# Kernel optimization log

Measured on AMD Instinct MI355X. Metric: run time of the kernel, lower is better.

Reference implementation:

```python
import jax, jax.numpy as jnp
import numpy as np

MIN_STD = 1e-05
LEAKY_SLOPE = 0.01


def setup_inputs() -> dict:
    key = jax.random.key(0)
    ks = jax.random.split(key, 8)
    T, B, F, H, A = 512, 256, 64, 256, 8
    s_in = 1.0 / np.sqrt(F)
    s_h = 1.0 / np.sqrt(H)
    return {
        "x": jax.random.normal(ks[0], (T, B, F), jnp.float32),
        "dones": jax.random.randint(ks[1], (T, B), 0, 2, jnp.int32),
        "W1": jax.random.normal(ks[2], (H, F), jnp.float32) * s_in,
        "b1": jnp.zeros((H,), jnp.float32),
        "W_ih": jax.random.normal(ks[3], (3 * H, H), jnp.float32) * s_h,
        "W_hh": jax.random.normal(ks[4], (3 * H, H), jnp.float32) * s_h,
        "b_ih": jnp.zeros((3 * H,), jnp.float32),
        "b_hh": jnp.zeros((3 * H,), jnp.float32),
        "Wm": jax.random.normal(ks[5], (A, H), jnp.float32) * s_h,
        "bm": jnp.zeros((A,), jnp.float32),
        "Ws": jax.random.normal(ks[6], (A, H), jnp.float32) * s_h,
        "bs": jnp.zeros((A,), jnp.float32),
    }


def reference(x, dones, W1, b1, W_ih, W_hh, b_ih, b_hh, Wm, bm, Ws, bs):
    T, B, _ = x.shape
    H = W1.shape[0]

    # shared_net: Linear + LeakyReLU, applied to the whole [T,B,F] tensor
    sf = jnp.einsum('tbf,hf->tbh', x, W1) + b1
    sf = jnp.where(sf >= 0, sf, LEAKY_SLOPE * sf)

    # per-timestep GRU with done-masked hidden reset (PyTorch gate order r,z,n)
    def step(h, inp):
        f_t, d_t = inp                      # f_t: [B,H], d_t: [B]
        h = jnp.where(d_t[:, None] > 0, 0.0, h)
        gi = f_t @ W_ih.T + b_ih            # [B,3H]
        gh = h @ W_hh.T + b_hh              # [B,3H]
        r = jax.nn.sigmoid(gi[:, :H] + gh[:, :H])
        z = jax.nn.sigmoid(gi[:, H:2 * H] + gh[:, H:2 * H])
        n = jnp.tanh(gi[:, 2 * H:] + r * gh[:, 2 * H:])
        h_new = (1.0 - z) * n + z * h
        return h_new, h_new

    h0 = jnp.zeros((B, H), x.dtype)
    h_final, outs = jax.lax.scan(step, h0, (sf, dones))

    # Faithful to source: heads applied to the LAST step's gru_output [1,B,H]
    last = outs[-1][None]                   # [1,B,H]
    means = jnp.tanh(jnp.einsum('sbh,ah->sba', last, Wm) + bm)
    stds = jax.nn.softplus(jnp.einsum('sbh,ah->sba', last, Ws) + bs)
    stds = jnp.maximum(stds, MIN_STD)
    hidden = h_final[None]                  # [num_layers=1, B, H]
    return means, stds, hidden
```

## Files before the change

### kernel.cpp

```cpp
#include <hip/hip_runtime.h>
#include <math.h>

typedef __attribute__((ext_vector_type(8))) _Float16 f16x8;
typedef __attribute__((ext_vector_type(4))) _Float16 f16x4;
typedef __attribute__((ext_vector_type(4))) float f32x4;

#define TT 512
#define BB 256
#define HH 256
#define AA 8

#define OFF_W1   0u
#define OFF_WIH  32768u
#define OFF_WHH  425984u
#define OFF_H    819200u
#define OFF_GI   1081344u
#define GSTRIDE  393216

__device__ inline float fexp2(float x) { return __builtin_amdgcn_exp2f(x); }
__device__ inline float frcp(float x)  { return __builtin_amdgcn_rcpf(x); }
__device__ inline float fsigm(float x) { return frcp(1.f + fexp2(x * -1.4426950408889634f)); }
__device__ inline float ftanh_(float x){ return 1.f - 2.f * frcp(1.f + fexp2(x * 2.8853900817779268f)); }

__global__ __launch_bounds__(256) void prepack(
    const float* __restrict__ W1, const float* __restrict__ Wih,
    const float* __restrict__ Whh, unsigned char* __restrict__ ws) {
  int gid = blockIdx.x * 256 + threadIdx.x;
  int wave = gid >> 6, l = gid & 63;
  const float* src; int K; int tix; size_t dst;
  if (wave < 32)       { src = W1;  K = 64;  tix = wave;       dst = OFF_W1; }
  else if (wave < 416) { src = Wih; K = 256; tix = wave - 32;  dst = OFF_WIH; }
  else                 { src = Whh; K = 256; tix = wave - 416; dst = OFF_WHH; }
  int ntJ = (K == 64) ? 16 : 48;
  int kt = tix / ntJ, jt = tix % ntJ;
  int j;
  if (K == 64) j = jt * 16 + (l & 15);
  else { int g = jt % 3, blk = jt / 3; j = g * 256 + blk * 16 + (l & 15); }
  int k = kt * 32 + (l >> 4) * 8;
  const float* p = src + (size_t)j * K + k;
  f16x8 frag;
#pragma unroll
  for (int e = 0; e < 8; ++e) frag[e] = (_Float16)p[e];
  *(f16x8*)(ws + dst + ((size_t)tix * 64 + l) * 16) = frag;
}

__global__ __launch_bounds__(256) void gru_gi(
    const float* __restrict__ x, const float* __restrict__ b1,
    const float* __restrict__ b_ih, const float* __restrict__ b_hh,
    const unsigned char* __restrict__ wsro, unsigned char* __restrict__ giout,
    int t0) {
  __shared__ __align__(16) _Float16 sfh[2][16 * 256];
  int tid = threadIdx.x, w = tid >> 6, l = tid & 63;
  int tp = blockIdx.x >> 4, bt = blockIdx.x & 15;
  int row = l & 15, kg = l >> 4;

  const f16x8* pW1 = (const f16x8*)(wsro + OFF_W1);
#pragma unroll
  for (int tt = 0; tt < 2; ++tt) {
    int t = t0 + tp * 2 + tt;
    f32x4 sacc[4] = {{0.f,0.f,0.f,0.f},{0.f,0.f,0.f,0.f},{0.f,0.f,0.f,0.f},{0.f,0.f,0.f,0.f}};
    size_t xbase = ((size_t)t * BB + bt * 16 + row) * 64;
#pragma unroll
    for (int kt = 0; kt < 2; ++kt) {
      float4 p0 = *(const float4*)(x + xbase + kt * 32 + kg * 8);
      float4 p1 = *(const float4*)(x + xbase + kt * 32 + kg * 8 + 4);
      float xv[8] = {p0.x, p0.y, p0.z, p0.w, p1.x, p1.y, p1.z, p1.w};
      f16x8 xh;
#pragma unroll
      for (int e = 0; e < 8; ++e) xh[e] = (_Float16)xv[e];
#pragma unroll
      for (int jj = 0; jj < 4; ++jj) {
        f16x8 bw = pW1[(kt * 16 + w * 4 + jj) * 64 + l];
        sacc[jj] = __builtin_amdgcn_mfma_f32_16x16x32_f16(xh, bw, sacc[jj], 0, 0, 0);
      }
    }
#pragma unroll
    for (int jj = 0; jj < 4; ++jj) {
      int j = (w * 4 + jj) * 16 + row;
      float b1v = b1[j];
#pragma unroll
      for (int rg = 0; rg < 4; ++rg) {
        int rr = kg * 4 + rg;
        float v = sacc[jj][rg] + b1v;
        v = v >= 0.f ? v : 0.01f * v;
        int byt = (j * 2) ^ ((rr & 7) << 4);
        *(_Float16*)((char*)sfh[tt] + rr * 512 + byt) = (_Float16)v;
      }
    }
  }
  __syncthreads();

  f32x4 gacc[2][12];
#pragma unroll
  for (int tt = 0; tt < 2; ++tt)
#pragma unroll
    for (int jj = 0; jj < 12; ++jj) gacc[tt][jj] = (f32x4){0.f, 0.f, 0.f, 0.f};
  const f16x8* pWih = (const f16x8*)(wsro + OFF_WIH);
  for (int kt = 0; kt < 8; ++kt) {
    int rb = row * 512 + ((kt * 64 + kg * 16) ^ ((row & 7) << 4));
    f16x8 ah0 = *(const f16x8*)((const char*)sfh[0] + rb);
    f16x8 ah1 = *(const f16x8*)((const char*)sfh[1] + rb);
#pragma unroll
    for (int jj = 0; jj < 12; ++jj) {
      f16x8 bw = pWih[((size_t)(kt * 48 + w * 12 + jj)) * 64 + l];
      gacc[0][jj] = __builtin_amdgcn_mfma_f32_16x16x32_f16(ah0, bw, gacc[0][jj], 0, 0, 0);
      gacc[1][jj] = __builtin_amdgcn_mfma_f32_16x16x32_f16(ah1, bw, gacc[1][jj], 0, 0, 0);
    }
  }
  float biasv[12];
#pragma unroll
  for (int jj = 0; jj < 12; ++jj) {
    int jt = w * 12 + jj;
    int g = jt % 3, blk = jt / 3;
    int j = g * 256 + blk * 16 + row;
    biasv[jj] = b_ih[j] + (g < 2 ? b_hh[j] : 0.f);
  }
#pragma unroll
  for (int tt = 0; tt < 2; ++tt) {
    unsigned char* gbase =
        giout + (size_t)((tp * 2 + tt) * 16 + bt) * 24576 + (l >> 5) * 12288;
#pragma unroll
    for (int jj = 0; jj < 12; ++jj) {
      int jt = w * 12 + jj;
      f16x4 o;
#pragma unroll
      for (int rg = 0; rg < 4; ++rg) o[rg] = (_Float16)(gacc[tt][jj][rg] + biasv[jj]);
      *(f16x4*)(gbase + jt * 256 + (l & 31) * 8) = o;
    }
  }
}

__global__ __launch_bounds__(512, 2) void gru_seq(
    const int* __restrict__ dones, const float* __restrict__ b_hh,
    const float* __restrict__ Wm, const float* __restrict__ bm,
    const float* __restrict__ Wsv, const float* __restrict__ bsv,
    const unsigned char* __restrict__ wsro, unsigned char* __restrict__ hcar,
    const unsigned char* __restrict__ gi, int t0, int tch,
    float* __restrict__ out) {
  __shared__ __align__(16) unsigned char hbuf[2][8192];
  __shared__ unsigned char dnb[2048];
  int tid = threadIdx.x, w = tid >> 6, u = tid & 63;
  int bt8 = blockIdx.x, bt16 = bt8 >> 1, half = bt8 & 1;
  int kg = u >> 4;
  int col16 = u & 15, rgrp = (u >> 4) & 1, blk = u >> 5;
  int c = (2 * w + blk) * 16 + col16;

  f16x8 whh[6][8];
  const f16x8* pWhh = (const f16x8*)(wsro + OFF_WHH);
#pragma unroll
  for (int jj = 0; jj < 6; ++jj)
#pragma unroll
    for (int kt = 0; kt < 8; ++kt)
      whh[jj][kt] = pWhh[(size_t)(kt * 48 + 6 * w + jj) * 64 + u];

  float bn = b_hh[512 + c];

  int ab0 = (kg * 256 + (u & 7) * 16) ^ (kg << 4);
  int ab1 = ab0 ^ 64;
  int ku2 = c >> 3, e2 = c & 7;
  int wbase = (ku2 * 256 + rgrp * 64 + e2 * 2) ^ ((ku2 & 7) << 4);
  const char* hro = (const char*)hbuf;

  {
    int buf = tid >> 8, r = tid & 255;
    f16x8 z;
#pragma unroll
    for (int e = 0; e < 8; ++e) z[e] = (_Float16)0.f;
    *(f16x8*)((char*)hbuf + buf * 8192 + (r >> 3) * 256 + 128 + (r & 7) * 16) = z;
  }

  float h_old[4];
#pragma unroll
  for (int rg = 0; rg < 4; ++rg) {
    float hv = ((const float*)hcar)[(bt8 * 8 + rgrp * 4 + rg) * 256 + c];
    h_old[rg] = hv;
    *(_Float16*)((char*)hbuf + (wbase ^ (rg << 4))) = (_Float16)hv;
  }

#pragma unroll
  for (int ii = 0; ii < 4; ++ii) {
    int ix = ii * 512 + tid;
    if (ix < tch * 8) {
      int ti = t0 + (ix >> 3) + 1;
      dnb[ix] = (ti < TT) ? (unsigned char)(dones[ti * BB + bt8 * 8 + (ix & 7)] != 0) : (unsigned char)0;
    }
  }

  const unsigned char* gpt = gi + (size_t)bt16 * 24576 + half * 12288 +
                             (2 * w + blk) * 768 + (u & 31) * 8;
  f16x4 gA[3], gB[3];
#pragma unroll
  for (int g = 0; g < 3; ++g) gA[g] = *(const f16x4*)(gpt + g * 256);

  asm volatile("s_waitcnt lgkmcnt(0)" ::: "memory");
  __builtin_amdgcn_s_barrier();

#define STEP(TL, P, GC, GN)                                                     \
  {                                                                             \
    int tn = (TL) + 1 < tch ? (TL) + 1 : tch - 1;                               \
    const unsigned char* gpn = gpt + (size_t)tn * GSTRIDE;                      \
    GN[0] = *(const f16x4*)(gpn);                                               \
    GN[1] = *(const f16x4*)(gpn + 256);                                         \
    GN[2] = *(const f16x4*)(gpn + 512);                                         \
    f32x4 acc[6];                                                               \
    _Pragma("unroll") for (int jj = 0; jj < 6; ++jj)                            \
        acc[jj] = (f32x4){0.f, 0.f, 0.f, 0.f};                                  \
    _Pragma("unroll") for (int kt = 0; kt < 8; ++kt) {                          \
      f16x8 ah = *(const f16x8*)(hro + (P) * 8192 + kt * 1024 +                 \
                                 ((kt & 1) ? ab1 : ab0));                       \
      _Pragma("unroll") for (int jj = 0; jj < 6; ++jj)                          \
        acc[jj] = __builtin_amdgcn_mfma_f32_16x16x32_f16(ah, whh[jj][kt],       \
                                                         acc[jj], 0, 0, 0);     \
    }                                                                           \
    int dn4 = *(const int*)(dnb + (TL) * 8 + rgrp * 4);                         \
    char* hw = (char*)hbuf + ((P) ^ 1) * 8192;                                  \
    _Pragma("unroll") for (int rg = 0; rg < 4; ++rg) {                          \
      float avr = blk ? acc[3][rg] : acc[0][rg];                                \
      float avz = blk ? acc[4][rg] : acc[1][rg];                                \
      float avn = blk ? acc[5][rg] : acc[2][rg];                                \
      float rs = fsigm((float)GC[0][rg] + avr);                                 \
      float zs = fsigm((float)GC[1][rg] + avz);                                 \
      float ng = ftanh_((float)GC[2][rg] + rs * (avn + bn));                    \
      float hn = ng + zs * (h_old[rg] - ng);                                    \
      hn = ((dn4 >> (rg * 8)) & 0xff) ? 0.f : hn;                               \
      h_old[rg] = hn;                                                           \
      *(_Float16*)(hw + (wbase ^ (rg << 4))) = (_Float16)hn;                    \
    }                                                                           \
    asm volatile("s_waitcnt lgkmcnt(0)" ::: "memory");                          \
    __builtin_amdgcn_s_barrier();                                               \
  }

  for (int tl = 0; tl < tch; tl += 2) {
    STEP(tl, 0, gA, gB);
    STEP(tl + 1, 1, gB, gA);
  }
#undef STEP

#pragma unroll
  for (int rg = 0; rg < 4; ++rg)
    ((float*)hcar)[(bt8 * 8 + rgrp * 4 + rg) * 256 + c] = h_old[rg];

  if (t0 + tch == TT) {
#pragma unroll
    for (int rg = 0; rg < 4; ++rg)
      out[2 * BB * AA + (bt8 * 8 + rgrp * 4 + rg) * 256 + c] = h_old[rg];
    if (tid < 128) {
      int r2 = tid >> 4, a = (tid >> 1) & 7, hd = tid & 1;
      const float* W = hd ? Wsv : Wm;
      float acc2 = 0.f;
      for (int k = 0; k < 256; k += 8) {
        int ku = k >> 3;
        f16x8 vh = *(const f16x8*)(hro + ((ku * 256 + r2 * 16) ^ ((ku & 7) << 4)));
#pragma unroll
        for (int e = 0; e < 8; ++e)
          acc2 += (float)vh[e] * W[a * 256 + k + e];
      }
      int b = bt8 * 8 + r2;
      if (hd == 0) {
        out[b * AA + a] = tanhf(acc2 + bm[a]);
      } else {
        float v = acc2 + bsv[a];
        float sp = fmaxf(v, 0.f) + log1pf(expf(-fabsf(v)));
        out[BB * AA + b * AA + a] = fmaxf(sp, 1e-5f);
      }
    }
  }
}

extern "C" void kernel_launch(void* const* d_in, const int* in_sizes, int n_in,
                              void* d_out, int out_size, void* d_ws, size_t ws_size,
                              hipStream_t stream) {
  const float* x    = (const float*)d_in[0];
  const int*   dn   = (const int*)  d_in[1];
  const float* W1   = (const float*)d_in[2];
  const float* b1   = (const float*)d_in[3];
  const float* W_ih = (const float*)d_in[4];
  const float* W_hh = (const float*)d_in[5];
  const float* b_ih = (const float*)d_in[6];
  const float* b_hh = (const float*)d_in[7];
  const float* Wm   = (const float*)d_in[8];
  const float* bm   = (const float*)d_in[9];
  const float* Wsv  = (const float*)d_in[10];
  const float* bs   = (const float*)d_in[11];
  float* out = (float*)d_out;
  unsigned char* ws = (unsigned char*)d_ws;

  int tch = 256;
  while (tch > 1 && (size_t)OFF_GI + (size_t)tch * 16 * 24576 > ws_size) tch >>= 1;

  prepack<<<200, 256, 0, stream>>>(W1, W_ih, W_hh, ws);
  (void)hipMemsetAsync(ws + OFF_H, 0, 262144, stream);
  for (int t0 = 0; t0 < TT; t0 += tch) {
    gru_gi<<<dim3((tch / 2) * 16), 256, 0, stream>>>(x, b1, b_ih, b_hh, ws, ws + OFF_GI, t0);
    gru_seq<<<32, 512, 0, stream>>>(dn, b_hh, Wm, bm, Wsv, bs, ws, ws + OFF_H,
                                    ws + OFF_GI, t0, tch, out);
  }
}
```

Baseline: 791.3 us.

## Overlap next chunk's input GEMM with sequential GRU recurrence in fused kernel

The input projection kernel and the sequential GRU kernel are fused into one launch. The first 32 blocks run the recurrence for the current time chunk, while the extra blocks compute the input-gate projections for the next chunk into a double-buffered workspace. This hides the parallel GEMM work behind the latency-bound recurrence, which only occupies 32 blocks. The costs are a smaller chunk size, twice the workspace, and the GEMM blocks possibly competing with the recurrent blocks for memory bandwidth and CU resources.

```diff
diff --git a/kernel.cpp b/kernel.cpp
--- a/kernel.cpp
+++ b/kernel.cpp
@@ -44,17 +44,14 @@
   *(f16x8*)(ws + dst + ((size_t)tix * 64 + l) * 16) = frag;
 }
 
-__global__ __launch_bounds__(256) void gru_gi(
+__device__ __forceinline__ void gi_sf_phase(
     const float* __restrict__ x, const float* __restrict__ b1,
-    const float* __restrict__ b_ih, const float* __restrict__ b_hh,
-    const unsigned char* __restrict__ wsro, unsigned char* __restrict__ giout,
-    int t0) {
-  __shared__ __align__(16) _Float16 sfh[2][16 * 256];
-  int tid = threadIdx.x, w = tid >> 6, l = tid & 63;
-  int tp = blockIdx.x >> 4, bt = blockIdx.x & 15;
+    const unsigned char* __restrict__ wsro, _Float16* sfh0, _Float16* sfh1,
+    int t0, int tp, int bt, int tid) {
+  int w = tid >> 6, l = tid & 63;
   int row = l & 15, kg = l >> 4;
-
   const f16x8* pW1 = (const f16x8*)(wsro + OFF_W1);
+  _Float16* sfh[2] = {sfh0, sfh1};
 #pragma unroll
   for (int tt = 0; tt < 2; ++tt) {
     int t = t0 + tp * 2 + tt;
@@ -88,8 +85,15 @@
       }
     }
   }
-  __syncthreads();
-
+}
+
+__device__ __forceinline__ void gi_gemm_phase(
+    const float* __restrict__ b_ih, const float* __restrict__ b_hh,
+    const unsigned char* __restrict__ wsro, const _Float16* sfh0,
+    const _Float16* sfh1, unsigned char* __restrict__ giout,
+    int tp, int bt, int tid) {
+  int w = tid >> 6, l = tid & 63;
+  int row = l & 15, kg = l >> 4;
   f32x4 gacc[2][12];
 #pragma unroll
   for (int tt = 0; tt < 2; ++tt)
@@ -98,8 +102,8 @@
   const f16x8* pWih = (const f16x8*)(wsro + OFF_WIH);
   for (int kt = 0; kt < 8; ++kt) {
     int rb = row * 512 + ((kt * 64 + kg * 16) ^ ((row & 7) << 4));
-    f16x8 ah0 = *(const f16x8*)((const char*)sfh[0] + rb);
-    f16x8 ah1 = *(const f16x8*)((const char*)sfh[1] + rb);
+    f16x8 ah0 = *(const f16x8*)((const char*)sfh0 + rb);
+    f16x8 ah1 = *(const f16x8*)((const char*)sfh1 + rb);
 #pragma unroll
     for (int jj = 0; jj < 12; ++jj) {
       f16x8 bw = pWih[((size_t)(kt * 48 + w * 12 + jj)) * 64 + l];
@@ -130,16 +134,46 @@
   }
 }
 
-__global__ __launch_bounds__(512, 2) void gru_seq(
-    const int* __restrict__ dones, const float* __restrict__ b_hh,
+__global__ __launch_bounds__(256) void gru_gi(
+    const float* __restrict__ x, const float* __restrict__ b1,
+    const float* __restrict__ b_ih, const float* __restrict__ b_hh,
+    const unsigned char* __restrict__ wsro, unsigned char* __restrict__ giout,
+    int t0) {
+  __shared__ __align__(16) _Float16 sfh[2][16 * 256];
+  int tid = threadIdx.x;
+  int tp = blockIdx.x >> 4, bt = blockIdx.x & 15;
+  gi_sf_phase(x, b1, wsro, sfh[0], sfh[1], t0, tp, bt, tid);
+  __syncthreads();
+  gi_gemm_phase(b_ih, b_hh, wsro, sfh[0], sfh[1], giout, tp, bt, tid);
+}
+
+__global__ __launch_bounds__(512, 2) void gru_fused(
+    const float* __restrict__ x,
+    const int* __restrict__ dones, const float* __restrict__ b1,
+    const float* __restrict__ b_ih, const float* __restrict__ b_hh,
     const float* __restrict__ Wm, const float* __restrict__ bm,
     const float* __restrict__ Wsv, const float* __restrict__ bsv,
     const unsigned char* __restrict__ wsro, unsigned char* __restrict__ hcar,
-    const unsigned char* __restrict__ gi, int t0, int tch,
+    const unsigned char* __restrict__ gi, unsigned char* __restrict__ giout,
+    int t0, int tch, int gi_t0,
     float* __restrict__ out) {
+  int tid = threadIdx.x;
+
+  if (blockIdx.x >= 32) {
+    __shared__ __align__(16) _Float16 sfh[2][16 * 256];
+    int bg = blockIdx.x - 32;
+    int tp = bg >> 4, bt = bg & 15;
+    if (tid < 256)
+      gi_sf_phase(x, b1, wsro, sfh[0], sfh[1], gi_t0, tp, bt, tid);
+    __syncthreads();
+    if (tid < 256)
+      gi_gemm_phase(b_ih, b_hh, wsro, sfh[0], sfh[1], giout, tp, bt, tid);
+    return;
+  }
+
   __shared__ __align__(16) unsigned char hbuf[2][8192];
   __shared__ unsigned char dnb[2048];
-  int tid = threadIdx.x, w = tid >> 6, u = tid & 63;
+  int w = tid >> 6, u = tid & 63;
   int bt8 = blockIdx.x, bt16 = bt8 >> 1, half = bt8 & 1;
   int kg = u >> 4;
   int col16 = u & 15, rgrp = (u >> 4) & 1, blk = u >> 5;
@@ -285,14 +319,24 @@
   float* out = (float*)d_out;
   unsigned char* ws = (unsigned char*)d_ws;
 
-  int tch = 256;
-  while (tch > 1 && (size_t)OFF_GI + (size_t)tch * 16 * 24576 > ws_size) tch >>= 1;
+  int tch = 128;
+  while (tch > 2 && (size_t)OFF_GI + 2 * (size_t)tch * 16 * 24576 > ws_size) tch >>= 1;
+  size_t GB = (size_t)tch * 16 * 24576;
+  int nch = TT / tch;
 
   prepack<<<200, 256, 0, stream>>>(W1, W_ih, W_hh, ws);
   (void)hipMemsetAsync(ws + OFF_H, 0, 262144, stream);
-  for (int t0 = 0; t0 < TT; t0 += tch) {
-    gru_gi<<<dim3((tch / 2) * 16), 256, 0, stream>>>(x, b1, b_ih, b_hh, ws, ws + OFF_GI, t0);
-    gru_seq<<<32, 512, 0, stream>>>(dn, b_hh, Wm, bm, Wsv, bs, ws, ws + OFF_H,
-                                    ws + OFF_GI, t0, tch, out);
-  }
-}
+
+  gru_gi<<<(tch / 2) * 16, 256, 0, stream>>>(x, b1, b_ih, b_hh, ws, ws + OFF_GI, 0);
+
+  for (int i = 0; i < nch; ++i) {
+    int t0 = i * tch;
+    int last = (i == nch - 1);
+    unsigned char* gin  = ws + OFF_GI + (size_t)(i & 1) * GB;
+    unsigned char* gout = ws + OFF_GI + (size_t)((i + 1) & 1) * GB;
+    int grid = 32 + (last ? 0 : (tch / 2) * 16);
+    gru_fused<<<grid, 512, 0, stream>>>(x, dn, b1, b_ih, b_hh, Wm, bm, Wsv, bs,
+                                        ws, ws + OFF_H, gin, gout,
+                                        t0, tch, t0 + tch, out);
+  }
+}
```

Measured after the change: 660.5 us. 16.5% less time.
